# Performance work log

Hardware: AMD Instinct MI355X
Metric: run time of the kernel (lower is better)

Reference implementation:

```python
import jax, jax.numpy as jnp
import numpy as np

IN_CH = 1024
HID_CH = 1024
NUM_HEADS = 16
HEAD_DIM = HID_CH // NUM_HEADS
SCALE = (HID_CH / NUM_HEADS) ** (-0.25)


def _xavier(key, shape):
    fan_out, fan_in = shape
    limit = np.sqrt(6.0 / (fan_in + fan_out)).astype(np.float32)
    return jax.random.uniform(key, shape, jnp.float32, -limit, limit)


def setup_inputs() -> dict:
    key = jax.random.key(0)
    ks = jax.random.split(key, 5)
    B, T, L = 4, 2048, 512
    inpt = jax.random.normal(ks[0], (B, IN_CH, T), jnp.float32)
    aux = jax.random.normal(ks[1], (L, IN_CH), jnp.float32)
    q_w = _xavier(ks[2], (HID_CH, IN_CH))
    q_b = jnp.zeros((HID_CH,), jnp.float32)
    kv_w = _xavier(ks[3], (2 * HID_CH, IN_CH))
    kv_b = jnp.zeros((2 * HID_CH,), jnp.float32)
    out_w = _xavier(ks[4], (IN_CH, HID_CH))
    out_b = jnp.zeros((IN_CH,), jnp.float32)
    return {"inpt": inpt, "aux": aux, "q_w": q_w, "q_b": q_b,
            "kv_w": kv_w, "kv_b": kv_b, "out_w": out_w, "out_b": out_b}


def reference(inpt, aux, q_w, q_b, kv_w, kv_b, out_w, out_b):
    # inpt: (B, C, T), aux: (L, C)
    B, C, T = inpt.shape
    x = jnp.swapaxes(inpt, -2, -1)                     # (B, T, C)
    q = (x @ q_w.T + q_b) * SCALE                      # (B, T, H*D)
    kv = aux @ kv_w.T + kv_b                           # (L, 2*H*D)
    k, v = jnp.split(kv, 2, axis=-1)
    k = k * SCALE
    q = q.reshape(B, T, NUM_HEADS, HEAD_DIM)           # (B, T, h, d)
    L = aux.shape[0]
    k = k.reshape(L, NUM_HEADS, HEAD_DIM)              # (L, h, d)
    v = v.reshape(L, NUM_HEADS, HEAD_DIM)
    e = jnp.einsum('bihd,jhd->bijh', q, k)             # (B, T, L, h)
    attn = jax.nn.softmax(e, axis=2)                   # softmax over key axis j
    out = jnp.einsum('bijh,jhd->bihd', attn, v)        # (B, T, h, d)
    out = out.reshape(B, T, HID_CH) @ out_w.T + out_b  # (B, T, C)
    return inpt + jnp.swapaxes(out, -2, -1)            # (B, C, T)
```

## Files before the change

### kernel.cpp

```cpp
#include <hip/hip_runtime.h>
#include <cstdint>
#include <cstddef>

typedef __bf16 bf16;
typedef __bf16 bf16x4 __attribute__((ext_vector_type(4)));
typedef __bf16 bf16x8 __attribute__((ext_vector_type(8)));
typedef float f32x4 __attribute__((ext_vector_type(4)));

static constexpr float SCALE_F = 0.35355339059327373f;

#define AS1 __attribute__((address_space(1)))
#define AS3 __attribute__((address_space(3)))

__device__ __forceinline__ void load_lds16(const void* g, void* l) {
  __builtin_amdgcn_global_load_lds((AS1 void*)g, (AS3 void*)l, 16, 0, 0);
}


__global__ void cvt_all(const float* __restrict__ a, bf16* __restrict__ oa,
                        const float* __restrict__ b, bf16* __restrict__ ob,
                        const float* __restrict__ c, bf16* __restrict__ oc,
                        const float* __restrict__ d, bf16* __restrict__ od) {
  int i = blockIdx.x * blockDim.x + threadIdx.x;
  const float* src;
  bf16* dst;
  int off;
  if (i < 262144) { src = a; dst = oa; off = i; }
  else if (i < 786432) { src = b; dst = ob; off = i - 262144; }
  else if (i < 1048576) { src = c; dst = oc; off = i - 786432; }
  else { src = d; dst = od; off = i - 1048576; }
  float4 v = reinterpret_cast<const float4*>(src)[off];
  bf16x4 o;
  o[0] = (bf16)v.x; o[1] = (bf16)v.y; o[2] = (bf16)v.z; o[3] = (bf16)v.w;
  reinterpret_cast<bf16x4*>(dst)[off] = o;
}

__global__ void transpose_in(const float* __restrict__ inpt, bf16* __restrict__ X) {
  __shared__ float tile[32][33];
  int b = blockIdx.z;
  int t0 = blockIdx.x * 32, c0 = blockIdx.y * 32;
  int tx = threadIdx.x, ty = threadIdx.y;
  const float* src = inpt + ((size_t)b * 1024 + c0) * 2048 + t0;
#pragma unroll
  for (int i = 0; i < 4; ++i) tile[ty + i * 8][tx] = src[(size_t)(ty + i * 8) * 2048 + tx];
  __syncthreads();
  bf16* dst = X + ((size_t)b * 2048 + t0) * 1024 + c0;
#pragma unroll
  for (int i = 0; i < 4; ++i) dst[(size_t)(ty + i * 8) * 1024 + tx] = (bf16)tile[tx][ty + i * 8];
}

__global__ void residual_out(const float* __restrict__ inpt, const bf16* __restrict__ Z,
                             float* __restrict__ out) {
  __shared__ float tile[32][33];
  int b = blockIdx.z;
  int t0 = blockIdx.x * 32, c0 = blockIdx.y * 32;
  int tx = threadIdx.x, ty = threadIdx.y;
  const bf16* zsrc = Z + ((size_t)b * 2048 + t0) * 1024 + c0;
#pragma unroll
  for (int i = 0; i < 4; ++i) tile[ty + i * 8][tx] = (float)zsrc[(size_t)(ty + i * 8) * 1024 + tx];
  __syncthreads();
  size_t ob = ((size_t)b * 1024 + c0) * 2048 + t0;
#pragma unroll
  for (int i = 0; i < 4; ++i) {
    size_t idx = ob + (size_t)(ty + i * 8) * 2048 + tx;
    out[idx] = inpt[idx] + tile[tx][ty + i * 8];
  }
}


__global__ __launch_bounds__(256, 2) void gemm_qkv(
    const bf16* __restrict__ X, const bf16* __restrict__ qwb, const float* __restrict__ q_b,
    bf16* __restrict__ Qout, const bf16* __restrict__ auxb, const bf16* __restrict__ kvwb,
    const float* __restrict__ kv_b, bf16* __restrict__ Kout, bf16* __restrict__ Vout) {
  __shared__ __align__(16) char sA[16384];
  __shared__ __align__(16) char sB[16384];
  const int tid = threadIdx.x;
  const int lane = tid & 63;
  const int wave = tid >> 6;
  const int wm = wave >> 1, wn = wave & 1;
  const int bid = blockIdx.x;
  const bool isQ = bid < 512;
  const bf16 *A, *Bw;
  const float* bias;
  int m0, n0;
  if (isQ) {
    A = X; Bw = qwb; bias = q_b;
    m0 = (bid >> 3) * 128; n0 = (bid & 7) * 128;
  } else {
    int b2 = bid - 512;
    A = auxb; Bw = kvwb; bias = kv_b;
    m0 = (b2 & 3) * 128; n0 = (b2 >> 2) * 128;
  }
  f32x4 acc[4][4] = {};

  for (int kt = 0; kt < 1024; kt += 64) {
#pragma unroll
    for (int j = 0; j < 4; ++j) {
      int i = tid + j * 256;
      int r = i >> 3, q = i & 7;
      int so = (q ^ (r & 7)) << 4;
      load_lds16((const char*)(A + (size_t)(m0 + r) * 1024 + kt) + so, sA + (size_t)i * 16);
      load_lds16((const char*)(Bw + (size_t)(n0 + r) * 1024 + kt) + so, sB + (size_t)i * 16);
    }
    asm volatile("s_waitcnt vmcnt(0)" ::: "memory");
    __syncthreads();
    bf16x8 af[4][2], bfr[4][2];
#pragma unroll
    for (int mi = 0; mi < 4; ++mi)
#pragma unroll
      for (int kk = 0; kk < 2; ++kk) {
        int rr = wm * 64 + mi * 16 + (lane & 15);
        int w = kk * 64 + ((lane >> 4) << 4);
        af[mi][kk] = *(const bf16x8*)(sA + (size_t)rr * 128 + (w ^ ((rr & 7) << 4)));
        int r2 = wn * 64 + mi * 16 + (lane & 15);
        bfr[mi][kk] = *(const bf16x8*)(sB + (size_t)r2 * 128 + (w ^ ((r2 & 7) << 4)));
      }
#pragma unroll
    for (int kk = 0; kk < 2; ++kk)
#pragma unroll
      for (int mi = 0; mi < 4; ++mi)
#pragma unroll
        for (int ni = 0; ni < 4; ++ni)
          acc[mi][ni] =
              __builtin_amdgcn_mfma_f32_16x16x32_bf16(af[mi][kk], bfr[ni][kk], acc[mi][ni], 0, 0, 0);
    __syncthreads();
  }

  float bs[4];
#pragma unroll
  for (int ni = 0; ni < 4; ++ni) bs[ni] = bias[n0 + wn * 64 + ni * 16 + (lane & 15)];

#pragma unroll
  for (int mi = 0; mi < 4; ++mi)
#pragma unroll
    for (int ni = 0; ni < 4; ++ni)
#pragma unroll
      for (int j = 0; j < 4; ++j) {
        int row = wm * 64 + mi * 16 + ((lane >> 4) << 2) + j;
        int col = wn * 64 + ni * 16 + (lane & 15);
        int m = m0 + row, n = n0 + col;
        float val = acc[mi][ni][j] + bs[ni];
        if (isQ) {
          val *= SCALE_F;
          int bb = m >> 11, t = m & 2047, hh = n >> 6, d = n & 63;
          Qout[(((size_t)(bb * 16 + hh) * 2048 + t) << 6) + d] = (bf16)val;
        } else {
          if (n < 1024) {
            int hh = n >> 6, d = n & 63;
            Kout[(((size_t)hh * 512 + m) << 6) + d] = (bf16)(val * SCALE_F);
          } else {
            int n2 = n - 1024;
            int hh = n2 >> 6, d = n2 & 63;
            int sl = (m & 0x1E0) | (((m >> 2) & 3) << 3) | (((m >> 4) & 1) << 2) | (m & 3);
            Vout[(((size_t)hh * 64 + d) << 9) + sl] = (bf16)val;
          }
        }
      }
}

__global__ __launch_bounds__(256, 2) void gemm_out(const bf16* __restrict__ A,
                                                   const bf16* __restrict__ Bw,
                                                   const float* __restrict__ bias,
                                                   bf16* __restrict__ out0) {
  __shared__ __align__(16) char sA[16384];
  __shared__ __align__(16) char sB[16384];
  const int tid = threadIdx.x;
  const int lane = tid & 63;
  const int wave = tid >> 6;
  const int wm = wave >> 1, wn = wave & 1;
  const int m0 = blockIdx.x * 128, n0 = blockIdx.y * 128;
  f32x4 acc[4][4] = {};

  for (int kt = 0; kt < 1024; kt += 64) {
#pragma unroll
    for (int j = 0; j < 4; ++j) {
      int i = tid + j * 256;
      int r = i >> 3, q = i & 7;
      int so = (q ^ (r & 7)) << 4;
      load_lds16((const char*)(A + (size_t)(m0 + r) * 1024 + kt) + so, sA + (size_t)i * 16);
      load_lds16((const char*)(Bw + (size_t)(n0 + r) * 1024 + kt) + so, sB + (size_t)i * 16);
    }
    asm volatile("s_waitcnt vmcnt(0)" ::: "memory");
    __syncthreads();
    bf16x8 af[4][2], bfr[4][2];
#pragma unroll
    for (int mi = 0; mi < 4; ++mi)
#pragma unroll
      for (int kk = 0; kk < 2; ++kk) {
        int rr = wm * 64 + mi * 16 + (lane & 15);
        int w = kk * 64 + ((lane >> 4) << 4);
        af[mi][kk] = *(const bf16x8*)(sA + (size_t)rr * 128 + (w ^ ((rr & 7) << 4)));
        int r2 = wn * 64 + mi * 16 + (lane & 15);
        bfr[mi][kk] = *(const bf16x8*)(sB + (size_t)r2 * 128 + (w ^ ((r2 & 7) << 4)));
      }
#pragma unroll
    for (int kk = 0; kk < 2; ++kk)
#pragma unroll
      for (int mi = 0; mi < 4; ++mi)
#pragma unroll
        for (int ni = 0; ni < 4; ++ni)
          acc[mi][ni] =
              __builtin_amdgcn_mfma_f32_16x16x32_bf16(af[mi][kk], bfr[ni][kk], acc[mi][ni], 0, 0, 0);
    __syncthreads();
  }

  float bs[4];
#pragma unroll
  for (int ni = 0; ni < 4; ++ni) bs[ni] = bias[n0 + wn * 64 + ni * 16 + (lane & 15)];
#pragma unroll
  for (int mi = 0; mi < 4; ++mi)
#pragma unroll
    for (int ni = 0; ni < 4; ++ni)
#pragma unroll
      for (int j = 0; j < 4; ++j) {
        int row = wm * 64 + mi * 16 + ((lane >> 4) << 2) + j;
        int col = wn * 64 + ni * 16 + (lane & 15);
        out0[(size_t)(m0 + row) * 1024 + n0 + col] = (bf16)(acc[mi][ni][j] + bs[ni]);
      }
}

struct Frags {
  bf16x8 ka[2][2];
  bf16x8 va[4];
};

__device__ __forceinline__ void load_frags(Frags& f, const char* lds, int G, int lr, int g) {
  const int swz = (lr & 7) << 4;
#pragma unroll
  for (int m = 0; m < 2; ++m)
#pragma unroll
    for (int kk = 0; kk < 2; ++kk)
      f.ka[m][kk] =
          *(const bf16x8*)(lds + (size_t)(G * 32 + m * 16 + lr) * 128 + ((kk * 64 + g * 16) ^ swz));
#pragma unroll
  for (int db = 0; db < 4; ++db)
    f.va[db] = *(const bf16x8*)(lds + 65536 + (size_t)(db * 16 + lr) * 1024 +
                                ((G * 64 + g * 16) ^ swz));
}

__device__ __forceinline__ void compute_group(const Frags& f, const bf16x8 (&qf)[4][2],
                                              f32x4 (&oacc)[4][4], float (&psum)[4]) {
  f32x4 sa[4][2] = {};
#pragma unroll
  for (int s = 0; s < 4; ++s)
#pragma unroll
    for (int m = 0; m < 2; ++m) {
      sa[s][m] = __builtin_amdgcn_mfma_f32_16x16x32_bf16(f.ka[m][0], qf[s][0], sa[s][m], 0, 0, 0);
      sa[s][m] = __builtin_amdgcn_mfma_f32_16x16x32_bf16(f.ka[m][1], qf[s][1], sa[s][m], 0, 0, 0);
    }
  bf16x8 pb[4];
#pragma unroll
  for (int s = 0; s < 4; ++s)
#pragma unroll
    for (int m = 0; m < 2; ++m)
#pragma unroll
      for (int j = 0; j < 4; ++j) {
        float p = __expf(sa[s][m][j] - 16.0f);
        psum[s] += p;
        pb[s][m * 4 + j] = (bf16)p;
      }
#pragma unroll
  for (int s = 0; s < 4; ++s)
#pragma unroll
    for (int db = 0; db < 4; ++db)
      oacc[s][db] = __builtin_amdgcn_mfma_f32_16x16x32_bf16(f.va[db], pb[s], oacc[s][db], 0, 0, 0);
}

__global__ __launch_bounds__(512, 2) void attn_kernel(const bf16* __restrict__ Q,
                                                      const bf16* __restrict__ Kw,
                                                      const bf16* __restrict__ Vt,
                                                      bf16* __restrict__ Y) {
  __shared__ __align__(16) char lds[131072];
  const int tid = threadIdx.x;
  const int lane = tid & 63;
  const int wv = tid >> 6;
  const int g = lane >> 4, lr = lane & 15;
  const int bix = blockIdx.x;
  const int b = bix >> 6, h = (bix >> 2) & 15, tc = bix & 3;

  const bf16* Kh = Kw + (size_t)h * 512 * 64;
  const bf16* Vh = Vt + (size_t)h * 64 * 512;
#pragma unroll
  for (int j = 0; j < 8; ++j) {
    int i = tid + j * 512;
    int r = i >> 3, c = i & 7;
    load_lds16((const char*)Kh + r * 128 + ((c * 16) ^ ((r & 7) << 4)), lds + (size_t)i * 16);
  }
#pragma unroll
  for (int j = 0; j < 8; ++j) {
    int i = tid + j * 512;
    int r = i >> 6, c = i & 63;
    load_lds16((const char*)Vh + r * 1024 + ((c * 16) ^ ((r & 7) << 4)),
               lds + 65536 + (size_t)i * 16);
  }

  const int tb = tc * 512 + wv * 64;
  const bf16* Qh = Q + ((size_t)(b * 16 + h) * 2048 + tb) * 64;
  bf16x8 qf[4][2];
#pragma unroll
  for (int s = 0; s < 4; ++s)
#pragma unroll
    for (int kk = 0; kk < 2; ++kk)
      qf[s][kk] = *(const bf16x8*)((const char*)Qh + (s * 16 + lr) * 128 + kk * 64 + g * 16);

  asm volatile("s_waitcnt vmcnt(0)" ::: "memory");
  __syncthreads();

  f32x4 oacc[4][4] = {};
  float psum[4] = {};

  Frags fA, fB;
  load_frags(fA, lds, 0, lr, g);
#pragma unroll 1
  for (int G = 0; G < 16; G += 2) {
    load_frags(fB, lds, G + 1, lr, g);
    compute_group(fA, qf, oacc, psum);
    if (G + 2 < 16) load_frags(fA, lds, G + 2, lr, g);
    compute_group(fB, qf, oacc, psum);
  }

#pragma unroll
  for (int s = 0; s < 4; ++s) {
    float ssum = psum[s];
    ssum += __shfl_xor(ssum, 16);
    ssum += __shfl_xor(ssum, 32);
    float inv = 1.0f / ssum;
    int t = tb + s * 16 + lr;
    char* yrow = (char*)Y + ((size_t)(b * 2048 + t) * 1024 + h * 64) * 2;
#pragma unroll
    for (int db = 0; db < 4; ++db) {
      bf16x4 w;
#pragma unroll
      for (int j = 0; j < 4; ++j) w[j] = (bf16)(oacc[s][db][j] * inv);
      *(bf16x4*)(yrow + (db * 16 + g * 4) * 2) = w;
    }
  }
}


extern "C" void kernel_launch(void* const* d_in, const int* in_sizes, int n_in, void* d_out,
                              int out_size, void* d_ws, size_t ws_size, hipStream_t stream) {
  const float* inpt = (const float*)d_in[0];
  const float* aux = (const float*)d_in[1];
  const float* q_w = (const float*)d_in[2];
  const float* q_b = (const float*)d_in[3];
  const float* kv_w = (const float*)d_in[4];
  const float* kv_b = (const float*)d_in[5];
  const float* out_w = (const float*)d_in[6];
  const float* out_b = (const float*)d_in[7];
  float* out = (float*)d_out;
  char* ws = (char*)d_ws;
  bf16* X = (bf16*)(ws + 0);
  bf16* QZ = (bf16*)(ws + (16u << 20));
  bf16* qwb = (bf16*)(ws + (32u << 20));
  bf16* kvwb = (bf16*)(ws + (34u << 20));
  bf16* owb = (bf16*)(ws + (38u << 20));
  bf16* auxb = (bf16*)(ws + (40u << 20));
  bf16* Kws = (bf16*)(ws + (41u << 20));
  bf16* Vtw = (bf16*)(ws + (42u << 20));

  cvt_all<<<4608, 256, 0, stream>>>(q_w, qwb, kv_w, kvwb, out_w, owb, aux, auxb);
  transpose_in<<<dim3(64, 32, 4), dim3(32, 8), 0, stream>>>(inpt, X);

  gemm_qkv<<<576, 256, 0, stream>>>(X, qwb, q_b, QZ, auxb, kvwb, kv_b, Kws, Vtw);
  attn_kernel<<<256, 512, 0, stream>>>(QZ, Kws, Vtw, X );
  gemm_out<<<dim3(64, 8), 256, 0, stream>>>(X, owb, out_b, QZ );
  residual_out<<<dim3(64, 32, 4), dim3(32, 8), 0, stream>>>(inpt, QZ, out);
}
```

Baseline: 205.6 us.

## Fuse residual transpose into output GEMM epilogue and merge prep kernels

Merges the weight conversion and input transpose into one prep launch. Fuses the residual add and transpose into the output GEMM epilogue: results are staged in a 64KB swizzled LDS tile, then written as coalesced fp32 rows with the input added. This removes the bf16 intermediate round trip through global memory and one launch. It also raises gemm_qkv launch bounds to 3 blocks per CU. The 64KB LDS can reduce gemm_out occupancy.

Measured after the change: 194.1 us. 1.06x faster.

```diff
diff --git a/kernel.cpp b/kernel.cpp
--- a/kernel.cpp
+++ b/kernel.cpp
@@ -16,59 +16,46 @@
   __builtin_amdgcn_global_load_lds((AS1 void*)g, (AS3 void*)l, 16, 0, 0);
 }
 
-
-__global__ void cvt_all(const float* __restrict__ a, bf16* __restrict__ oa,
-                        const float* __restrict__ b, bf16* __restrict__ ob,
-                        const float* __restrict__ c, bf16* __restrict__ oc,
-                        const float* __restrict__ d, bf16* __restrict__ od) {
-  int i = blockIdx.x * blockDim.x + threadIdx.x;
-  const float* src;
-  bf16* dst;
-  int off;
-  if (i < 262144) { src = a; dst = oa; off = i; }
-  else if (i < 786432) { src = b; dst = ob; off = i - 262144; }
-  else if (i < 1048576) { src = c; dst = oc; off = i - 786432; }
-  else { src = d; dst = od; off = i - 1048576; }
-  float4 v = reinterpret_cast<const float4*>(src)[off];
-  bf16x4 o;
-  o[0] = (bf16)v.x; o[1] = (bf16)v.y; o[2] = (bf16)v.z; o[3] = (bf16)v.w;
-  reinterpret_cast<bf16x4*>(dst)[off] = o;
-}
-
-__global__ void transpose_in(const float* __restrict__ inpt, bf16* __restrict__ X) {
-  __shared__ float tile[32][33];
-  int b = blockIdx.z;
-  int t0 = blockIdx.x * 32, c0 = blockIdx.y * 32;
-  int tx = threadIdx.x, ty = threadIdx.y;
-  const float* src = inpt + ((size_t)b * 1024 + c0) * 2048 + t0;
-#pragma unroll
-  for (int i = 0; i < 4; ++i) tile[ty + i * 8][tx] = src[(size_t)(ty + i * 8) * 2048 + tx];
-  __syncthreads();
-  bf16* dst = X + ((size_t)b * 2048 + t0) * 1024 + c0;
-#pragma unroll
-  for (int i = 0; i < 4; ++i) dst[(size_t)(ty + i * 8) * 1024 + tx] = (bf16)tile[tx][ty + i * 8];
-}
-
-__global__ void residual_out(const float* __restrict__ inpt, const bf16* __restrict__ Z,
-                             float* __restrict__ out) {
-  __shared__ float tile[32][33];
-  int b = blockIdx.z;
-  int t0 = blockIdx.x * 32, c0 = blockIdx.y * 32;
-  int tx = threadIdx.x, ty = threadIdx.y;
-  const bf16* zsrc = Z + ((size_t)b * 2048 + t0) * 1024 + c0;
-#pragma unroll
-  for (int i = 0; i < 4; ++i) tile[ty + i * 8][tx] = (float)zsrc[(size_t)(ty + i * 8) * 1024 + tx];
-  __syncthreads();
-  size_t ob = ((size_t)b * 1024 + c0) * 2048 + t0;
-#pragma unroll
-  for (int i = 0; i < 4; ++i) {
-    size_t idx = ob + (size_t)(ty + i * 8) * 2048 + tx;
-    out[idx] = inpt[idx] + tile[tx][ty + i * 8];
-  }
-}
-
-
-__global__ __launch_bounds__(256, 2) void gemm_qkv(
+__global__ void prep(const float* __restrict__ q_w, bf16* __restrict__ qwb,
+                     const float* __restrict__ kv_w, bf16* __restrict__ kvwb,
+                     const float* __restrict__ out_w, bf16* __restrict__ owb,
+                     const float* __restrict__ aux, bf16* __restrict__ auxb,
+                     const float* __restrict__ inpt, bf16* __restrict__ X) {
+  const int bid = blockIdx.x;
+  const int tid = threadIdx.x;
+  if (bid < 4608) {
+    int i = bid * 256 + tid;
+    const float* src;
+    bf16* dst;
+    int off;
+    if (i < 262144) { src = q_w; dst = qwb; off = i; }
+    else if (i < 786432) { src = kv_w; dst = kvwb; off = i - 262144; }
+    else if (i < 1048576) { src = out_w; dst = owb; off = i - 786432; }
+    else { src = aux; dst = auxb; off = i - 1048576; }
+    float4 v = reinterpret_cast<const float4*>(src)[off];
+    bf16x4 o;
+    o[0] = (bf16)v.x; o[1] = (bf16)v.y; o[2] = (bf16)v.z; o[3] = (bf16)v.w;
+    reinterpret_cast<bf16x4*>(dst)[off] = o;
+  } else {
+    __shared__ float tile[32][33];
+    int tb = bid - 4608;
+    int b = tb >> 11;
+    int rem = tb & 2047;
+    int c0 = (rem >> 6) * 32;
+    int t0 = (rem & 63) * 32;
+    int tx = tid & 31, ty = tid >> 5;
+    const float* src = inpt + ((size_t)b * 1024 + c0) * 2048 + t0;
+#pragma unroll
+    for (int i = 0; i < 4; ++i) tile[ty + i * 8][tx] = src[(size_t)(ty + i * 8) * 2048 + tx];
+    __syncthreads();
+    bf16* dst = X + ((size_t)b * 2048 + t0) * 1024 + c0;
+#pragma unroll
+    for (int i = 0; i < 4; ++i) dst[(size_t)(ty + i * 8) * 1024 + tx] = (bf16)tile[tx][ty + i * 8];
+  }
+}
+
+
+__global__ __launch_bounds__(256, 3) void gemm_qkv(
     const bf16* __restrict__ X, const bf16* __restrict__ qwb, const float* __restrict__ q_b,
     bf16* __restrict__ Qout, const bf16* __restrict__ auxb, const bf16* __restrict__ kvwb,
     const float* __restrict__ kv_b, bf16* __restrict__ Kout, bf16* __restrict__ Vout) {
@@ -158,16 +145,19 @@
       }
 }
 
-__global__ __launch_bounds__(256, 2) void gemm_out(const bf16* __restrict__ A,
-                                                   const bf16* __restrict__ Bw,
-                                                   const float* __restrict__ bias,
-                                                   bf16* __restrict__ out0) {
-  __shared__ __align__(16) char sA[16384];
-  __shared__ __align__(16) char sB[16384];
+__global__ __launch_bounds__(256, 2) void gemm_outres(const bf16* __restrict__ A,
+                                                      const bf16* __restrict__ Bw,
+                                                      const float* __restrict__ bias,
+                                                      const float* __restrict__ inpt,
+                                                      float* __restrict__ out) {
+  __shared__ __align__(16) char smem[65536];
+  char* sA = smem;
+  char* sB = smem + 16384;
   const int tid = threadIdx.x;
   const int lane = tid & 63;
   const int wave = tid >> 6;
   const int wm = wave >> 1, wn = wave & 1;
+  const int g = lane >> 4, lr = lane & 15;
   const int m0 = blockIdx.x * 128, n0 = blockIdx.y * 128;
   f32x4 acc[4][4] = {};
 
@@ -187,10 +177,10 @@
     for (int mi = 0; mi < 4; ++mi)
 #pragma unroll
       for (int kk = 0; kk < 2; ++kk) {
-        int rr = wm * 64 + mi * 16 + (lane & 15);
-        int w = kk * 64 + ((lane >> 4) << 4);
+        int rr = wm * 64 + mi * 16 + lr;
+        int w = kk * 64 + (g << 4);
         af[mi][kk] = *(const bf16x8*)(sA + (size_t)rr * 128 + (w ^ ((rr & 7) << 4)));
-        int r2 = wn * 64 + mi * 16 + (lane & 15);
+        int r2 = wn * 64 + mi * 16 + lr;
         bfr[mi][kk] = *(const bf16x8*)(sB + (size_t)r2 * 128 + (w ^ ((r2 & 7) << 4)));
       }
 #pragma unroll
@@ -206,17 +196,39 @@
 
   float bs[4];
 #pragma unroll
-  for (int ni = 0; ni < 4; ++ni) bs[ni] = bias[n0 + wn * 64 + ni * 16 + (lane & 15)];
+  for (int ni = 0; ni < 4; ++ni) bs[ni] = bias[n0 + wn * 64 + ni * 16 + lr];
+
 #pragma unroll
   for (int mi = 0; mi < 4; ++mi)
 #pragma unroll
-    for (int ni = 0; ni < 4; ++ni)
-#pragma unroll
-      for (int j = 0; j < 4; ++j) {
-        int row = wm * 64 + mi * 16 + ((lane >> 4) << 2) + j;
-        int col = wn * 64 + ni * 16 + (lane & 15);
-        out0[(size_t)(m0 + row) * 1024 + n0 + col] = (bf16)(acc[mi][ni][j] + bs[ni]);
-      }
+    for (int ni = 0; ni < 4; ++ni) {
+      int c_l = wn * 64 + ni * 16 + lr;
+      int tb = (wm * 64 + mi * 16 + g * 4) * 4;
+      f32x4 v;
+#pragma unroll
+      for (int j = 0; j < 4; ++j) v[j] = acc[mi][ni][j] + bs[ni];
+      *(f32x4*)(smem + (size_t)c_l * 512 + (tb ^ ((c_l & 31) << 4))) = v;
+    }
+  __syncthreads();
+
+  const int c_r = tid >> 3;
+  const int tcol = (tid & 7) * 16;
+  const int b = m0 >> 11, m0t = m0 & 2047;
+#pragma unroll
+  for (int p = 0; p < 4; ++p) {
+    int c = p * 32 + c_r;
+    size_t grow = ((size_t)b * 1024 + n0 + c) * 2048 + m0t;
+#pragma unroll
+    for (int q = 0; q < 4; ++q) {
+      int t = tcol + q * 128;
+      f32x4 z = *(const f32x4*)(smem + (size_t)c * 512 + (t ^ ((c & 31) << 4)));
+      f32x4 iv = *(const f32x4*)(inpt + grow + (t >> 2));
+      f32x4 w;
+#pragma unroll
+      for (int j = 0; j < 4; ++j) w[j] = iv[j] + z[j];
+      *(f32x4*)(out + grow + (t >> 2)) = w;
+    }
+  }
 }
 
 struct Frags {
@@ -359,11 +371,8 @@
   bf16* Kws = (bf16*)(ws + (41u << 20));
   bf16* Vtw = (bf16*)(ws + (42u << 20));
 
-  cvt_all<<<4608, 256, 0, stream>>>(q_w, qwb, kv_w, kvwb, out_w, owb, aux, auxb);
-  transpose_in<<<dim3(64, 32, 4), dim3(32, 8), 0, stream>>>(inpt, X);
-
+  prep<<<12800, 256, 0, stream>>>(q_w, qwb, kv_w, kvwb, out_w, owb, aux, auxb, inpt, X);
   gemm_qkv<<<576, 256, 0, stream>>>(X, qwb, q_b, QZ, auxb, kvwb, kv_b, Kws, Vtw);
   attn_kernel<<<256, 512, 0, stream>>>(QZ, Kws, Vtw, X );
-  gemm_out<<<dim3(64, 8), 256, 0, stream>>>(X, owb, out_b, QZ );
-  residual_out<<<dim3(64, 32, 4), dim3(32, 8), 0, stream>>>(inpt, QZ, out);
-}
+  gemm_outres<<<dim3(64, 8), 256, 0, stream>>>(X, owb, out_b, inpt, out);
+}
```
